# Kernel optimization log

Hardware: AMD Instinct MI355X
Metric: run time of the kernel (lower is better)

The kernel has to match this reference:

```python
import jax, jax.numpy as jnp
import numpy as np

N_NODES = 100000
N_EDGES = 640000
D_IN = 128
D_OUT = 128

def setup_inputs() -> dict:
    key = jax.random.key(0)
    k1, k2, k3, k4, k5 = jax.random.split(key, 5)
    feat = jax.random.normal(k1, (N_NODES, D_IN), dtype=jnp.float32)
    src = jax.random.randint(k2, (N_EDGES,), 0, N_NODES, dtype=jnp.int32)
    dst = jax.random.randint(k3, (N_EDGES,), 0, N_NODES, dtype=jnp.int32)
    scale = 1.0 / np.sqrt(D_IN)
    W_self = jax.random.normal(k4, (D_IN, D_OUT), dtype=jnp.float32) * scale
    W_neigh = jax.random.normal(k5, (D_IN, D_OUT), dtype=jnp.float32) * scale
    b_self = jnp.zeros((D_OUT,), dtype=jnp.float32)
    b_neigh = jnp.zeros((D_OUT,), dtype=jnp.float32)
    return {"feat": feat, "src": src, "dst": dst,
            "W_self": W_self, "b_self": b_self,
            "W_neigh": W_neigh, "b_neigh": b_neigh}

def reference(feat, src, dst, W_self, b_self, W_neigh, b_neigh):
    # GraphSAGE 'mean' aggregator: copy_src + mean reduce over in-edges, then
    # rst = fc_self(h_self) + fc_neigh(h_neigh). feat_drop=0, no activation/norm.
    n = feat.shape[0]
    msg = feat[src]                                   # [E, D_in] gather
    neigh_sum = jax.ops.segment_sum(msg, dst, num_segments=n)      # [N, D_in]
    deg = jax.ops.segment_sum(jnp.ones_like(dst, dtype=feat.dtype), dst,
                              num_segments=n)          # [N]
    # mean with zero-in-degree nodes -> 0 (DGL semantics)
    h_neigh = neigh_sum / jnp.maximum(deg, 1.0)[:, None]
    rst = feat @ W_self + b_self + h_neigh @ W_neigh + b_neigh      # [N, D_out]
    return rst
```

## Files before the change

kernel.cpp:

```cpp
#include <hip/hip_runtime.h>


constexpr int N_NODES = 100000;
constexpr int N_EDGES = 640000;
constexpr int D = 128;

constexpr int SCAN_NBLOCKS = 98;

typedef __attribute__((ext_vector_type(8))) short bf16x8;
typedef __attribute__((ext_vector_type(4))) float f32x4;

__device__ __forceinline__ unsigned short f2bf(float f) {
    unsigned int u = __float_as_uint(f);
    unsigned int r = u + 0x7FFFu + ((u >> 16) & 1u);
    return (unsigned short)(r >> 16);
}

__global__ __launch_bounds__(256) void zero_deg_kernel(int4* __restrict__ deg4) {
    int i = blockIdx.x * 256 + threadIdx.x;
    if (i < N_NODES / 4) deg4[i] = int4{0, 0, 0, 0};
}

__global__ void prepass_kernel(const int* __restrict__ dst, int* __restrict__ deg,
                               const float* __restrict__ Ws, const float* __restrict__ Wn,
                               unsigned short* __restrict__ wp,
                               const float* __restrict__ feat, unsigned short* __restrict__ fb,
                               int* __restrict__ ctr) {
    const int gid = blockIdx.x * blockDim.x + threadIdx.x;
    if (gid == 0) ctr[0] = 0;
    if (gid < N_EDGES) atomicAdd(&deg[dst[gid]], 1);
    if (gid < 2 * D * D) {
        int i = gid;
        int r  = i & 7;
        int c  = (i >> 3) & 127;
        int h  = (i >> 10) & 3;
        int ks = (i >> 12) & 3;
        int m  = i >> 14;
        const float* W = m ? Wn : Ws;
        int k = ks * 32 + h * 8 + r;
        wp[i] = f2bf(W[k * D + c]);
    }
    const int total4 = N_NODES * D / 4;
    for (int i = gid; i < total4; i += N_EDGES) {
        float4 v = ((const float4*)feat)[i];
        ushort4 o;
        o.x = f2bf(v.x); o.y = f2bf(v.y); o.z = f2bf(v.z); o.w = f2bf(v.w);
        ((ushort4*)fb)[i] = o;
    }
}

__global__ __launch_bounds__(256) void scan_kernel(const int* __restrict__ deg,
                                                   int* __restrict__ rowptr,
                                                   int* __restrict__ cursor,
                                                   int* __restrict__ bsum,
                                                   int* __restrict__ ctr) {
    __shared__ int wsum[4];
    const int tid = threadIdx.x;
    const int lane = tid & 63;
    const int wave = tid >> 6;
    const int base = (blockIdx.x * 256 + tid) * 4;

    int local[4];
    int tsum = 0;
    #pragma unroll
    for (int j = 0; j < 4; j++) {
        int idx = base + j;
        local[j] = (idx < N_NODES) ? deg[idx] : 0;
        tsum += local[j];
    }
    {
        int s = tsum;
        for (int off = 32; off > 0; off >>= 1) s += __shfl_down(s, off, 64);
        if (lane == 0) wsum[wave] = s;
        __syncthreads();
        if (tid == 0) bsum[blockIdx.x] = wsum[0] + wsum[1] + wsum[2] + wsum[3];
    }
    __syncthreads();
    if (tid == 0) {
        __threadfence();
        __hip_atomic_fetch_add(ctr, 1, __ATOMIC_ACQ_REL, __HIP_MEMORY_SCOPE_AGENT);
        while (__hip_atomic_load(ctr, __ATOMIC_ACQUIRE, __HIP_MEMORY_SCOPE_AGENT)
               < SCAN_NBLOCKS) {}
    }
    __syncthreads();

    int v = (tid < blockIdx.x) ? bsum[tid] : 0;
    for (int off = 32; off > 0; off >>= 1) v += __shfl_down(v, off, 64);
    if (lane == 0) wsum[wave] = v;
    __syncthreads();
    const int boff = wsum[0] + wsum[1] + wsum[2] + wsum[3];
    __syncthreads();

    int incl = tsum;
    for (int off = 1; off < 64; off <<= 1) {
        int u = __shfl_up(incl, off, 64);
        if (lane >= off) incl += u;
    }
    if (lane == 63) wsum[wave] = incl;
    __syncthreads();
    int woff = 0;
    for (int w = 0; w < 4; w++) woff += (w < wave) ? wsum[w] : 0;

    int run = boff + woff + (incl - tsum);
    #pragma unroll
    for (int j = 0; j < 4; j++) {
        int idx = base + j;
        if (idx < N_NODES) {
            rowptr[idx] = run;
            cursor[idx] = run;
            run += local[j];
        }
    }
    if (blockIdx.x == 0 && tid == 0) rowptr[N_NODES] = N_EDGES;
}

__global__ void fill_kernel(const int* __restrict__ src, const int* __restrict__ dst,
                            int* __restrict__ cursor, int* __restrict__ csr_src) {
    int e = blockIdx.x * blockDim.x + threadIdx.x;
    if (e < N_EDGES) {
        int pos = atomicAdd(&cursor[dst[e]], 1);
        csr_src[pos] = src[e];
    }
}

__global__ __launch_bounds__(256) void gather_kernel(
    const unsigned short* __restrict__ fb, const int* __restrict__ csr_src,
    const int* __restrict__ rowptr, unsigned short* __restrict__ hn)
{
    const int lane = threadIdx.x & 63;
    const int n = (blockIdx.x * blockDim.x + threadIdx.x) >> 6;
    if (n >= N_NODES) return;

    const int e0 = rowptr[n];
    const int e1 = rowptr[n + 1];

    float ax = 0.f, ay = 0.f;
    for (int base = e0; base < e1; base += 8) {
        int sidx[8];
        #pragma unroll
        for (int j = 0; j < 8; j++) {
            int ee = base + j;
            ee = (ee < e1) ? ee : (e1 - 1);
            sidx[j] = csr_src[ee];
        }
        unsigned int v[8];
        #pragma unroll
        for (int j = 0; j < 8; j++)
            v[j] = ((const unsigned int*)(fb + (size_t)sidx[j] * D))[lane];
        #pragma unroll
        for (int j = 0; j < 8; j++) {
            const float w = (base + j < e1) ? 1.0f : 0.0f;
            ax = fmaf(w, __uint_as_float(v[j] << 16), ax);
            ay = fmaf(w, __uint_as_float(v[j] & 0xFFFF0000u), ay);
        }
    }
    const float sc = 1.0f / (float)max(e1 - e0, 1);
    const unsigned int packed =
        ((unsigned int)f2bf(ay * sc) << 16) | (unsigned int)f2bf(ax * sc);
    ((unsigned int*)(hn + (size_t)n * D))[lane] = packed;
}

__global__ __launch_bounds__(256) void mmfused_kernel(
    const unsigned short* __restrict__ fb, const unsigned short* __restrict__ hn,
    const unsigned short* __restrict__ wp,
    const float* __restrict__ b_self, const float* __restrict__ b_neigh,
    float* __restrict__ out)
{
    const int tid = threadIdx.x;
    const int wave = tid >> 6, lane = tid & 63;
    const int h = lane >> 4, c = lane & 15;
    const int row_base = blockIdx.x * 128 + wave * 32;

    bf16x8 a[2][2][4];
    #pragma unroll
    for (int ti = 0; ti < 2; ti++) {
        int row = row_base + ti * 16 + c;
        int rowc = min(row, N_NODES - 1);
        const bf16x8* f0 = (const bf16x8*)(fb + (size_t)rowc * D);
        const bf16x8* f1 = (const bf16x8*)(hn + (size_t)rowc * D);
        #pragma unroll
        for (int ks = 0; ks < 4; ks++) {
            a[0][ti][ks] = f0[ks * 4 + h];
            a[1][ti][ks] = f1[ks * 4 + h];
        }
    }

    const bf16x8* wpv = (const bf16x8*)wp;
    for (int ct = 0; ct < 8; ct++) {
        f32x4 acc[2];
        #pragma unroll
        for (int ti = 0; ti < 2; ti++) acc[ti] = f32x4{0.f, 0.f, 0.f, 0.f};

        #pragma unroll
        for (int m = 0; m < 2; m++) {
            bf16x8 b[4];
            #pragma unroll
            for (int ks = 0; ks < 4; ks++)
                b[ks] = wpv[((m * 4 + ks) * 4 + h) * 128 + ct * 16 + c];
            #pragma unroll
            for (int ks = 0; ks < 4; ks++)
                #pragma unroll
                for (int ti = 0; ti < 2; ti++)
                    acc[ti] = __builtin_amdgcn_mfma_f32_16x16x32_bf16(a[m][ti][ks], b[ks], acc[ti], 0, 0, 0);
        }

        const int col = ct * 16 + c;
        const float bias = b_self[col] + b_neigh[col];
        #pragma unroll
        for (int ti = 0; ti < 2; ti++) {
            if (row_base + ti * 16 < N_NODES) {
                #pragma unroll
                for (int q = 0; q < 4; q++) {
                    int row = row_base + ti * 16 + h * 4 + q;
                    __builtin_nontemporal_store(acc[ti][q] + bias,
                                                &out[(size_t)row * D + col]);
                }
            }
        }
    }
}

extern "C" void kernel_launch(void* const* d_in, const int* in_sizes, int n_in,
                              void* d_out, int out_size, void* d_ws, size_t ws_size,
                              hipStream_t stream) {
    const float* feat    = (const float*)d_in[0];
    const int*   src     = (const int*)d_in[1];
    const int*   dst     = (const int*)d_in[2];
    const float* W_self  = (const float*)d_in[3];
    const float* b_self  = (const float*)d_in[4];
    const float* W_neigh = (const float*)d_in[5];
    const float* b_neigh = (const float*)d_in[6];
    float* out = (float*)d_out;

    unsigned short* fb = (unsigned short*)d_ws;
    unsigned short* hn = fb + (size_t)N_NODES * D;
    unsigned short* wp = hn + (size_t)N_NODES * D;
    int*   deg     = (int*)(wp + 2 * D * D);
    int*   rowptr  = deg + N_NODES;
    int*   cursor  = rowptr + (N_NODES + 1);
    int*   csr_src = cursor + N_NODES;
    int*   bsum    = csr_src + N_EDGES;
    int*   ctr     = bsum + SCAN_NBLOCKS;

    zero_deg_kernel<<<(N_NODES / 4 + 255) / 256, 256, 0, stream>>>((int4*)deg);

    prepass_kernel<<<(N_EDGES + 255) / 256, 256, 0, stream>>>(dst, deg, W_self, W_neigh,
                                                              wp, feat, fb, ctr);

    scan_kernel<<<SCAN_NBLOCKS, 256, 0, stream>>>(deg, rowptr, cursor, bsum, ctr);

    fill_kernel<<<(N_EDGES + 255) / 256, 256, 0, stream>>>(src, dst, cursor, csr_src);

    gather_kernel<<<25000, 256, 0, stream>>>(fb, csr_src, rowptr, hn);

    mmfused_kernel<<<(N_NODES + 127) / 128, 256, 0, stream>>>(fb, hn, wp, b_self, b_neigh, out);
}
```

Before: 139.1 us.

## Fuse degree count into scan via grid barrier and merge feature conversion into fill

The kernel pipeline is restructured. Zeroing and weight packing now share one small kernel. The degree histogram runs inside the scan kernel, separated from the scan by a second software grid barrier over 98 persistent blocks. The feature-to-bf16 conversion moves from the prepass into the CSR fill kernel, and several loads use nontemporal hints. The aim is to cut launch count and to overlap the conversion with the atomic fill. In exchange, the degree atomics run on only 98 blocks, which may be slower than the previous wide launch.

```diff
diff --git a/kernel.cpp b/kernel.cpp
--- a/kernel.cpp
+++ b/kernel.cpp
@@ -16,20 +16,15 @@
     return (unsigned short)(r >> 16);
 }
 
-__global__ __launch_bounds__(256) void zero_deg_kernel(int4* __restrict__ deg4) {
-    int i = blockIdx.x * 256 + threadIdx.x;
-    if (i < N_NODES / 4) deg4[i] = int4{0, 0, 0, 0};
-}
-
-__global__ void prepass_kernel(const int* __restrict__ dst, int* __restrict__ deg,
-                               const float* __restrict__ Ws, const float* __restrict__ Wn,
-                               unsigned short* __restrict__ wp,
-                               const float* __restrict__ feat, unsigned short* __restrict__ fb,
-                               int* __restrict__ ctr) {
-    const int gid = blockIdx.x * blockDim.x + threadIdx.x;
-    if (gid == 0) ctr[0] = 0;
-    if (gid < N_EDGES) atomicAdd(&deg[dst[gid]], 1);
-    if (gid < 2 * D * D) {
+__global__ __launch_bounds__(256) void zero_kernel(int4* __restrict__ deg4,
+                                                   int* __restrict__ ctr,
+                                                   const float* __restrict__ Ws,
+                                                   const float* __restrict__ Wn,
+                                                   unsigned short* __restrict__ wp) {
+    const int gid = blockIdx.x * 256 + threadIdx.x;
+    if (gid < N_NODES / 4) deg4[gid] = int4{0, 0, 0, 0};
+    if (gid < 2) ctr[gid] = 0;
+    {
         int i = gid;
         int r  = i & 7;
         int c  = (i >> 3) & 127;
@@ -40,32 +35,44 @@
         int k = ks * 32 + h * 8 + r;
         wp[i] = f2bf(W[k * D + c]);
     }
-    const int total4 = N_NODES * D / 4;
-    for (int i = gid; i < total4; i += N_EDGES) {
-        float4 v = ((const float4*)feat)[i];
-        ushort4 o;
-        o.x = f2bf(v.x); o.y = f2bf(v.y); o.z = f2bf(v.z); o.w = f2bf(v.w);
-        ((ushort4*)fb)[i] = o;
-    }
-}
-
-__global__ __launch_bounds__(256) void scan_kernel(const int* __restrict__ deg,
-                                                   int* __restrict__ rowptr,
-                                                   int* __restrict__ cursor,
-                                                   int* __restrict__ bsum,
-                                                   int* __restrict__ ctr) {
+}
+
+__device__ __forceinline__ void grid_barrier(int* ctr) {
+    __syncthreads();
+    if (threadIdx.x == 0) {
+        __threadfence();
+        __hip_atomic_fetch_add(ctr, 1, __ATOMIC_ACQ_REL, __HIP_MEMORY_SCOPE_AGENT);
+        while (__hip_atomic_load(ctr, __ATOMIC_ACQUIRE, __HIP_MEMORY_SCOPE_AGENT)
+               < SCAN_NBLOCKS) {}
+    }
+    __syncthreads();
+}
+
+__global__ __launch_bounds__(256) void csrscan_kernel(const int* __restrict__ dst,
+                                                      int* __restrict__ deg,
+                                                      int* __restrict__ rowptr,
+                                                      int* __restrict__ cursor,
+                                                      int* __restrict__ bsum,
+                                                      int* __restrict__ ctr) {
     __shared__ int wsum[4];
     const int tid = threadIdx.x;
     const int lane = tid & 63;
     const int wave = tid >> 6;
+
+    for (int e = blockIdx.x * 256 + tid; e < N_EDGES; e += SCAN_NBLOCKS * 256)
+        atomicAdd(&deg[dst[e]], 1);
+
+    grid_barrier(&ctr[0]);
+
     const int base = (blockIdx.x * 256 + tid) * 4;
-
     int local[4];
     int tsum = 0;
     #pragma unroll
     for (int j = 0; j < 4; j++) {
         int idx = base + j;
-        local[j] = (idx < N_NODES) ? deg[idx] : 0;
+        local[j] = (idx < N_NODES)
+            ? __hip_atomic_load(&deg[idx], __ATOMIC_RELAXED, __HIP_MEMORY_SCOPE_AGENT)
+            : 0;
         tsum += local[j];
     }
     {
@@ -75,17 +82,12 @@
         __syncthreads();
         if (tid == 0) bsum[blockIdx.x] = wsum[0] + wsum[1] + wsum[2] + wsum[3];
     }
-    __syncthreads();
-    if (tid == 0) {
-        __threadfence();
-        __hip_atomic_fetch_add(ctr, 1, __ATOMIC_ACQ_REL, __HIP_MEMORY_SCOPE_AGENT);
-        while (__hip_atomic_load(ctr, __ATOMIC_ACQUIRE, __HIP_MEMORY_SCOPE_AGENT)
-               < SCAN_NBLOCKS) {}
-    }
-    __syncthreads();
+
+    grid_barrier(&ctr[1]);
 
     int v = (tid < blockIdx.x) ? bsum[tid] : 0;
     for (int off = 32; off > 0; off >>= 1) v += __shfl_down(v, off, 64);
+    __syncthreads();
     if (lane == 0) wsum[wave] = v;
     __syncthreads();
     const int boff = wsum[0] + wsum[1] + wsum[2] + wsum[3];
@@ -114,12 +116,22 @@
     if (blockIdx.x == 0 && tid == 0) rowptr[N_NODES] = N_EDGES;
 }
 
-__global__ void fill_kernel(const int* __restrict__ src, const int* __restrict__ dst,
-                            int* __restrict__ cursor, int* __restrict__ csr_src) {
-    int e = blockIdx.x * blockDim.x + threadIdx.x;
-    if (e < N_EDGES) {
-        int pos = atomicAdd(&cursor[dst[e]], 1);
-        csr_src[pos] = src[e];
+__global__ void fillcvt_kernel(const int* __restrict__ src, const int* __restrict__ dst,
+                               int* __restrict__ cursor, int* __restrict__ csr_src,
+                               const float* __restrict__ feat,
+                               unsigned short* __restrict__ fb) {
+    const int gid = blockIdx.x * blockDim.x + threadIdx.x;
+    if (gid < N_EDGES) {
+        int pos = atomicAdd(&cursor[dst[gid]], 1);
+        csr_src[pos] = src[gid];
+    }
+    const int total4 = N_NODES * D / 4;
+    const f32x4* fv = (const f32x4*)feat;
+    for (int i = gid; i < total4; i += N_EDGES) {
+        f32x4 v = __builtin_nontemporal_load(&fv[i]);
+        ushort4 o;
+        o.x = f2bf(v.x); o.y = f2bf(v.y); o.z = f2bf(v.z); o.w = f2bf(v.w);
+        ((ushort4*)fb)[i] = o;
     }
 }
 
@@ -180,8 +192,8 @@
         const bf16x8* f1 = (const bf16x8*)(hn + (size_t)rowc * D);
         #pragma unroll
         for (int ks = 0; ks < 4; ks++) {
-            a[0][ti][ks] = f0[ks * 4 + h];
-            a[1][ti][ks] = f1[ks * 4 + h];
+            a[0][ti][ks] = __builtin_nontemporal_load(&f0[ks * 4 + h]);
+            a[1][ti][ks] = __builtin_nontemporal_load(&f1[ks * 4 + h]);
         }
     }
 
@@ -242,14 +254,12 @@
     int*   bsum    = csr_src + N_EDGES;
     int*   ctr     = bsum + SCAN_NBLOCKS;
 
-    zero_deg_kernel<<<(N_NODES / 4 + 255) / 256, 256, 0, stream>>>((int4*)deg);
-
-    prepass_kernel<<<(N_EDGES + 255) / 256, 256, 0, stream>>>(dst, deg, W_self, W_neigh,
-                                                              wp, feat, fb, ctr);
-
-    scan_kernel<<<SCAN_NBLOCKS, 256, 0, stream>>>(deg, rowptr, cursor, bsum, ctr);
-
-    fill_kernel<<<(N_EDGES + 255) / 256, 256, 0, stream>>>(src, dst, cursor, csr_src);
+    zero_kernel<<<128, 256, 0, stream>>>((int4*)deg, ctr, W_self, W_neigh, wp);
+
+    csrscan_kernel<<<SCAN_NBLOCKS, 256, 0, stream>>>(dst, deg, rowptr, cursor, bsum, ctr);
+
+    fillcvt_kernel<<<(N_EDGES + 255) / 256, 256, 0, stream>>>(src, dst, cursor, csr_src,
+                                                              feat, fb);
 
     gather_kernel<<<25000, 256, 0, stream>>>(fb, csr_src, rowptr, hn);
 
```

Result: slower. 170.1 us (+22.3%).
